# Kernel optimization log

Hardware: AMD Instinct MI355X
Metric: run time of the kernel (lower is better)

## Reference

```python
import jax, jax.numpy as jnp
import numpy as np

DIM_MODEL = 512
HEADS = 8
DIM_HEAD = 64
HIDDEN = HEADS * DIM_HEAD
SCALE = DIM_HEAD ** -0.5
GN_EPS = 1e-5


def setup_inputs() -> dict:
    key = jax.random.key(0)
    ks = jax.random.split(key, 7)
    b, t = 8, 4096
    x = jax.random.normal(ks[0], (b, DIM_MODEL, t), dtype=jnp.float32)
    mask = jax.random.randint(ks[1], (b, t), 0, 2) == 1  # bool padding mask
    # 1x1 convs are plain channel matmuls; kernels squeezed to 2D
    w_qkv = jax.random.normal(ks[2], (3 * HIDDEN, DIM_MODEL), dtype=jnp.float32) * (DIM_MODEL ** -0.5)
    w_out = jax.random.normal(ks[3], (DIM_MODEL, HIDDEN), dtype=jnp.float32) * (HIDDEN ** -0.5)
    b_out = jax.random.normal(ks[4], (DIM_MODEL,), dtype=jnp.float32) * 0.01
    gn_gamma = jnp.ones((DIM_MODEL,), dtype=jnp.float32)
    gn_beta = jnp.zeros((DIM_MODEL,), dtype=jnp.float32)
    return {"x": x, "mask": mask, "w_qkv": w_qkv, "w_out": w_out,
            "b_out": b_out, "gn_gamma": gn_gamma, "gn_beta": gn_beta}


def reference(x, mask, w_qkv, w_out, b_out, gn_gamma, gn_beta):
    b, c, t = x.shape
    # to_qkv: 1x1 conv == channel matmul -> [b, 3*hidden, t]
    qkv = jnp.einsum('oc,bct->bot', w_qkv, x)
    q, k, v = jnp.split(qkv, 3, axis=1)
    # 'b (h d) t -> b h d t'
    q = q.reshape(b, HEADS, DIM_HEAD, t)
    k = k.reshape(b, HEADS, DIM_HEAD, t)
    v = v.reshape(b, HEADS, DIM_HEAD, t)
    # additive mask: 0.0 where True, 1e-12 where False; broadcast 'b t -> b 1 1 t'
    maskf = jnp.where(mask, 0.0, 1e-12)[:, None, None, :].astype(x.dtype)
    q = jax.nn.softmax(q, axis=-2) * SCALE            # softmax over feature dim d
    k = jax.nn.softmax(k + maskf, axis=-1)            # softmax over time dim t
    # linear attention: O(t * d * e)
    context = jnp.einsum('bhdn,bhen->bhde', k, v)      # [b, h, d, e]
    out = jnp.einsum('bhde,bhdn->bhen', context, q)    # [b, h, e, t]
    out = out.reshape(b, HIDDEN, t)                    # 'b h e t -> b (h e) t'
    # to_out: 1x1 conv with bias, then GroupNorm(1, dim_model)
    y = jnp.einsum('oc,bct->bot', w_out, out) + b_out[None, :, None]
    mu = jnp.mean(y, axis=(1, 2), keepdims=True)
    var = jnp.var(y, axis=(1, 2), keepdims=True)
    y = (y - mu) * jax.lax.rsqrt(var + GN_EPS)
    return y * gn_gamma[None, :, None] + gn_beta[None, :, None]
```

## Files before the change

### kernel.cpp

```cpp
#include <hip/hip_runtime.h>
#include <stdint.h>

typedef unsigned short u16;
using f32x4 = __attribute__((ext_vector_type(4))) float;
using s16x8 = __attribute__((ext_vector_type(8))) short;

#define MFMA_BF16(a, b, c) __builtin_amdgcn_mfma_f32_16x16x32_bf16((a), (b), (c), 0, 0, 0)

#define GLOAD_LDS16(gptr, lptr)                                                               \
  __builtin_amdgcn_global_load_lds((const __attribute__((address_space(1))) uint32_t*)(gptr), \
                                   (__attribute__((address_space(3))) uint32_t*)(lptr), 16, 0, 0)

__device__ __forceinline__ u16 f2bf(float f) {
  union { float f; uint32_t u; } v; v.f = f;
  uint32_t r = v.u + 0x7fffu + ((v.u >> 16) & 1u);
  return (u16)(r >> 16);
}
__device__ __forceinline__ float bf2f(u16 h) {
  union { uint32_t u; float f; } v; v.u = ((uint32_t)h) << 16;
  return v.f;
}

__global__ void k_convert_w(const float* __restrict__ wq, const float* __restrict__ wo,
                            u16* __restrict__ wqb, u16* __restrict__ wob) {
  int i = blockIdx.x * 256 + threadIdx.x;
  const int nq = 1536 * 512 / 4;
  const int no = 512 * 512 / 4;
  if (i < nq) {
    float4 v = ((const float4*)wq)[i];
    u16* o = wqb + i * 4;
    o[0] = f2bf(v.x); o[1] = f2bf(v.y); o[2] = f2bf(v.z); o[3] = f2bf(v.w);
  } else if (i < nq + no) {
    int j = i - nq;
    float4 v = ((const float4*)wo)[j];
    u16* o = wob + j * 4;
    o[0] = f2bf(v.x); o[1] = f2bf(v.y); o[2] = f2bf(v.z); o[3] = f2bf(v.w);
  }
}

__global__ void k_transpose_x(const float* __restrict__ x, u16* __restrict__ xT) {
  __shared__ u16 tile[64][65];
  int b = blockIdx.z, c0 = blockIdx.y * 64, t0 = blockIdx.x * 64;
  const float* xp = x + ((size_t)b * 512 + c0) * 4096 + t0;
#pragma unroll
  for (int i = 0; i < 16; ++i) {
    int idx = threadIdx.x + i * 256;
    int r = idx >> 6, col = idx & 63;
    tile[r][col] = f2bf(xp[(size_t)r * 4096 + col]);
  }
  __syncthreads();
  u16* op = xT + ((size_t)b * 4096 + t0) * 512 + c0;
#pragma unroll
  for (int i = 0; i < 16; ++i) {
    int idx = threadIdx.x + i * 256;
    int r = idx >> 6, col = idx & 63;
    op[(size_t)r * 512 + col] = tile[col][r];
  }
}

__launch_bounds__(256, 2)
__global__ void k_gemm_qkv(const u16* __restrict__ A, const u16* __restrict__ BT,
                           u16* __restrict__ C, u16* __restrict__ qT) {
  __shared__ s16x8 As8[1024];
  __shared__ s16x8 Bs8[1024];
  int b = blockIdx.z;
  int m0 = blockIdx.y * 128, n0 = blockIdx.x * 128;
  const u16* Ab = A + (size_t)m0 * 512;
  const u16* Bb = BT + ((size_t)b * 4096 + n0) * 512;
  int tid = threadIdx.x, w = tid >> 6, lane = tid & 63;
  int wm = (w >> 1) * 64, wn = (w & 1) * 64;
  f32x4 acc[4][4] = {};
  for (int kt = 0; kt < 8; ++kt) {
    if (kt) __syncthreads();
#pragma unroll
    for (int it = 0; it < 4; ++it) {
      int L = (w * 4 + it) * 64 + lane;
      int r = L >> 3;
      int lc = (L & 7) ^ (r & 7);
      GLOAD_LDS16(Ab + (size_t)r * 512 + kt * 64 + lc * 8, ((char*)As8) + (w * 4 + it) * 1024);
      GLOAD_LDS16(Bb + (size_t)r * 512 + kt * 64 + lc * 8, ((char*)Bs8) + (w * 4 + it) * 1024);
    }
    asm volatile("s_waitcnt vmcnt(0)");
    __syncthreads();
#pragma unroll
    for (int kk = 0; kk < 2; ++kk) {
      int cb = kk * 4 + (lane >> 4);
      s16x8 af[4], bfr[4];
#pragma unroll
      for (int mi = 0; mi < 4; ++mi) {
        int r = wm + mi * 16 + (lane & 15);
        af[mi] = As8[r * 8 + (cb ^ (r & 7))];
      }
#pragma unroll
      for (int ni = 0; ni < 4; ++ni) {
        int r = wn + ni * 16 + (lane & 15);
        bfr[ni] = Bs8[r * 8 + (cb ^ (r & 7))];
      }
#pragma unroll
      for (int mi = 0; mi < 4; ++mi)
#pragma unroll
        for (int ni = 0; ni < 4; ++ni)
          acc[mi][ni] = MFMA_BF16(af[mi], bfr[ni], acc[mi][ni]);
    }
  }
  if (blockIdx.y < 4) {
    int head = (m0 >> 6) + (wm >> 6);
    int bh = b * 8 + head;
#pragma unroll
    for (int ni = 0; ni < 4; ++ni) {
      float mx = -1e30f;
#pragma unroll
      for (int mi = 0; mi < 4; ++mi)
#pragma unroll
        for (int j = 0; j < 4; ++j) mx = fmaxf(mx, acc[mi][ni][j]);
      mx = fmaxf(mx, __shfl_xor(mx, 16));
      mx = fmaxf(mx, __shfl_xor(mx, 32));
      float e[4][4];
      float s = 0.f;
#pragma unroll
      for (int mi = 0; mi < 4; ++mi)
#pragma unroll
        for (int j = 0; j < 4; ++j) { e[mi][j] = __expf(acc[mi][ni][j] - mx); s += e[mi][j]; }
      s += __shfl_xor(s, 16);
      s += __shfl_xor(s, 32);
      float sc = 0.125f / s;
      int t = n0 + wn + ni * 16 + (lane & 15);
      u16* op = qT + ((size_t)bh * 4096 + t) * 64 + (lane >> 4) * 4;
#pragma unroll
      for (int mi = 0; mi < 4; ++mi) {
        union { u16 u[4]; uint2 v; } pk;
#pragma unroll
        for (int j = 0; j < 4; ++j) pk.u[j] = f2bf(e[mi][j] * sc);
        *(uint2*)(op + mi * 16) = pk.v;
      }
    }
  } else {
    u16* Cb = C + ((size_t)b * 1536 + m0) * 4096 + n0;
#pragma unroll
    for (int mi = 0; mi < 4; ++mi)
#pragma unroll
      for (int ni = 0; ni < 4; ++ni)
#pragma unroll
        for (int j = 0; j < 4; ++j) {
          int mm = wm + mi * 16 + (lane >> 4) * 4 + j;
          int nn = wn + ni * 16 + (lane & 15);
          Cb[(size_t)mm * 4096 + nn] = f2bf(acc[mi][ni][j]);
        }
  }
}

__global__ void k_softmax_k(u16* __restrict__ kp) {
  int row = blockIdx.x;
  int b = row >> 9, rem = row & 511;
  u16* p = kp + ((size_t)b * 1536 + 512 + rem) * 4096;
  int tid = threadIdx.x, lane = tid & 63, w = tid >> 6;
  s16x8 c0 = ((const s16x8*)p)[tid];
  s16x8 c1 = ((const s16x8*)p)[tid + 256];
  float v[16];
#pragma unroll
  for (int j = 0; j < 8; ++j) { v[j] = bf2f((u16)c0[j]); v[8 + j] = bf2f((u16)c1[j]); }
  float mx = -1e30f;
#pragma unroll
  for (int j = 0; j < 16; ++j) mx = fmaxf(mx, v[j]);
#pragma unroll
  for (int off = 32; off; off >>= 1) mx = fmaxf(mx, __shfl_xor(mx, off));
  __shared__ float redm[4], reds[4];
  if (lane == 0) redm[w] = mx;
  __syncthreads();
  mx = fmaxf(fmaxf(redm[0], redm[1]), fmaxf(redm[2], redm[3]));
  float s = 0.f;
#pragma unroll
  for (int j = 0; j < 16; ++j) { v[j] = __expf(v[j] - mx); s += v[j]; }
#pragma unroll
  for (int off = 32; off; off >>= 1) s += __shfl_xor(s, off);
  if (lane == 0) reds[w] = s;
  __syncthreads();
  s = reds[0] + reds[1] + reds[2] + reds[3];
  float inv = 1.f / s;
  s16x8 o0, o1;
#pragma unroll
  for (int j = 0; j < 8; ++j) { o0[j] = (short)f2bf(v[j] * inv); o1[j] = (short)f2bf(v[8 + j] * inv); }
  ((s16x8*)p)[tid] = o0;
  ((s16x8*)p)[tid + 256] = o1;
}

__global__ void k_context_part(const u16* __restrict__ qkv, float* __restrict__ part) {
  int s = blockIdx.x;
  int bh = blockIdx.y;
  int b = bh >> 3, h = bh & 7;
  const u16* vbase = qkv + ((size_t)b * 1536 + 1024 + h * 64) * 4096 + s * 256;
  const u16* kbase = qkv + ((size_t)b * 1536 + 512 + h * 64) * 4096 + s * 256;
  int w = threadIdx.x >> 6, lane = threadIdx.x & 63;
  int e0 = w * 16;
  f32x4 acc[4] = {};
  int er = e0 + (lane & 15);
  int nl = (lane >> 4) * 8;
#pragma unroll
  for (int n0 = 0; n0 < 256; n0 += 32) {
    s16x8 a = *(const s16x8*)(vbase + (size_t)er * 4096 + n0 + nl);
#pragma unroll
    for (int ni = 0; ni < 4; ++ni) {
      s16x8 bb = *(const s16x8*)(kbase + (size_t)(ni * 16 + (lane & 15)) * 4096 + n0 + nl);
      acc[ni] = MFMA_BF16(a, bb, acc[ni]);
    }
  }
  float* cp = part + ((size_t)bh * 16 + s) * 4096;
#pragma unroll
  for (int ni = 0; ni < 4; ++ni)
#pragma unroll
    for (int j = 0; j < 4; ++j) {
      int e = e0 + (lane >> 4) * 4 + j;
      int d = ni * 16 + (lane & 15);
      cp[e * 64 + d] = acc[ni][j];
    }
}

__global__ void k_context_reduce(const float* __restrict__ part, u16* __restrict__ ctxT) {
  int idx = blockIdx.x * 256 + threadIdx.x;
  int bh = idx >> 12, ed = idx & 4095;
  const float* pp = part + (size_t)bh * 16 * 4096 + ed;
  float sum = 0.f;
#pragma unroll
  for (int s = 0; s < 16; ++s) sum += pp[(size_t)s * 4096];
  ctxT[(size_t)bh * 4096 + ed] = f2bf(sum);
}

__launch_bounds__(256, 2)
__global__ void k_attn_out(const u16* __restrict__ qT, const u16* __restrict__ ctxT,
                           u16* __restrict__ outT) {
  __shared__ s16x8 Qs[1024];
  __shared__ s16x8 Cs[512];
  int bh = blockIdx.y;
  int t0 = blockIdx.x * 128;
  int b = bh >> 3, h = bh & 7;
  const u16* qb = qT + ((size_t)bh * 4096 + t0) * 64;
  const u16* cb = ctxT + (size_t)bh * 64 * 64;
  int tid = threadIdx.x, w = tid >> 6, lane = tid & 63;
#pragma unroll
  for (int it = 0; it < 4; ++it) {
    int L = (w * 4 + it) * 64 + lane;
    int r = L >> 3, lc = (L & 7) ^ (r & 7);
    GLOAD_LDS16(qb + (size_t)r * 64 + lc * 8, ((char*)Qs) + (w * 4 + it) * 1024);
  }
#pragma unroll
  for (int it = 0; it < 2; ++it) {
    int L = (w * 2 + it) * 64 + lane;
    int r = L >> 3, lc = (L & 7) ^ (r & 7);
    GLOAD_LDS16(cb + (size_t)r * 64 + lc * 8, ((char*)Cs) + (w * 2 + it) * 1024);
  }
  asm volatile("s_waitcnt vmcnt(0)");
  __syncthreads();
  f32x4 acc[2][4] = {};
#pragma unroll
  for (int kk = 0; kk < 2; ++kk) {
    int cbi = kk * 4 + (lane >> 4);
    s16x8 af[2], bfr[4];
#pragma unroll
    for (int mi = 0; mi < 2; ++mi) {
      int r = w * 32 + mi * 16 + (lane & 15);
      af[mi] = Qs[r * 8 + (cbi ^ (r & 7))];
    }
#pragma unroll
    for (int ni = 0; ni < 4; ++ni) {
      int r = ni * 16 + (lane & 15);
      bfr[ni] = Cs[r * 8 + (cbi ^ (r & 7))];
    }
#pragma unroll
    for (int mi = 0; mi < 2; ++mi)
#pragma unroll
      for (int ni = 0; ni < 4; ++ni)
        acc[mi][ni] = MFMA_BF16(af[mi], bfr[ni], acc[mi][ni]);
  }
  u16* op = outT + ((size_t)b * 4096 + t0) * 512 + h * 64;
#pragma unroll
  for (int mi = 0; mi < 2; ++mi)
#pragma unroll
    for (int ni = 0; ni < 4; ++ni)
#pragma unroll
      for (int j = 0; j < 4; ++j) {
        int t = w * 32 + mi * 16 + (lane >> 4) * 4 + j;
        int e = ni * 16 + (lane & 15);
        op[(size_t)t * 512 + e] = f2bf(acc[mi][ni][j]);
      }
}

__launch_bounds__(256, 2)
__global__ void k_gemm_wout(const u16* __restrict__ A, const u16* __restrict__ BT,
                            u16* __restrict__ Ybf, const float* __restrict__ bias,
                            float2* __restrict__ part2) {
  __shared__ s16x8 As8[1024];
  __shared__ s16x8 Bs8[1024];
  int b = blockIdx.z;
  int m0 = blockIdx.y * 128, n0 = blockIdx.x * 128;
  const u16* Ab = A + (size_t)m0 * 512;
  const u16* Bb = BT + ((size_t)b * 4096 + n0) * 512;
  int tid = threadIdx.x, w = tid >> 6, lane = tid & 63;
  int wm = (w >> 1) * 64, wn = (w & 1) * 64;
  f32x4 acc[4][4] = {};
  for (int kt = 0; kt < 8; ++kt) {
    if (kt) __syncthreads();
#pragma unroll
    for (int it = 0; it < 4; ++it) {
      int L = (w * 4 + it) * 64 + lane;
      int r = L >> 3;
      int lc = (L & 7) ^ (r & 7);
      GLOAD_LDS16(Ab + (size_t)r * 512 + kt * 64 + lc * 8, ((char*)As8) + (w * 4 + it) * 1024);
      GLOAD_LDS16(Bb + (size_t)r * 512 + kt * 64 + lc * 8, ((char*)Bs8) + (w * 4 + it) * 1024);
    }
    asm volatile("s_waitcnt vmcnt(0)");
    __syncthreads();
#pragma unroll
    for (int kk = 0; kk < 2; ++kk) {
      int cb = kk * 4 + (lane >> 4);
      s16x8 af[4], bfr[4];
#pragma unroll
      for (int mi = 0; mi < 4; ++mi) {
        int r = wm + mi * 16 + (lane & 15);
        af[mi] = As8[r * 8 + (cb ^ (r & 7))];
      }
#pragma unroll
      for (int ni = 0; ni < 4; ++ni) {
        int r = wn + ni * 16 + (lane & 15);
        bfr[ni] = Bs8[r * 8 + (cb ^ (r & 7))];
      }
#pragma unroll
      for (int mi = 0; mi < 4; ++mi)
#pragma unroll
        for (int ni = 0; ni < 4; ++ni)
          acc[mi][ni] = MFMA_BF16(af[mi], bfr[ni], acc[mi][ni]);
    }
  }
  u16* Yb = Ybf + ((size_t)b * 512 + m0) * 4096 + n0;
  float sm = 0.f, ssm = 0.f;
#pragma unroll
  for (int mi = 0; mi < 4; ++mi)
#pragma unroll
    for (int j = 0; j < 4; ++j) {
      int mm = wm + mi * 16 + (lane >> 4) * 4 + j;
      float bo = bias[m0 + mm];
#pragma unroll
      for (int ni = 0; ni < 4; ++ni) {
        int nn = wn + ni * 16 + (lane & 15);
        float vv = acc[mi][ni][j] + bo;
        sm += vv;
        ssm += vv * vv;
        Yb[(size_t)mm * 4096 + nn] = f2bf(vv);
      }
    }
#pragma unroll
  for (int off = 32; off; off >>= 1) { sm += __shfl_xor(sm, off); ssm += __shfl_xor(ssm, off); }
  __shared__ float sr[4], ssr[4];
  if (lane == 0) { sr[w] = sm; ssr[w] = ssm; }
  __syncthreads();
  if (tid == 0) {
    float2 o;
    o.x = sr[0] + sr[1] + sr[2] + sr[3];
    o.y = ssr[0] + ssr[1] + ssr[2] + ssr[3];
    part2[((size_t)b * 4 + blockIdx.y) * 32 + blockIdx.x] = o;
  }
}

__global__ void k_gn_norm(const u16* __restrict__ ybf, float* __restrict__ y,
                          const float2* __restrict__ part2,
                          const float* __restrict__ gamma, const float* __restrict__ beta) {
  int b = blockIdx.y;
  float s = 0.f, ss = 0.f;
#pragma unroll 8
  for (int i = 0; i < 128; ++i) { float2 pp = part2[b * 128 + i]; s += pp.x; ss += pp.y; }
  const float N = 512.f * 4096.f;
  float mu = s / N;
  float var = ss / N - mu * mu;
  float rstd = rsqrtf(var + 1e-5f);
  size_t base = ((size_t)b << 21) + (size_t)blockIdx.x * 16384;
  const s16x8* ip = (const s16x8*)(ybf + base);
  float4* opf = (float4*)(y + base);
#pragma unroll
  for (int i = 0; i < 8; ++i) {
    int idx = threadIdx.x + i * 256;
    int loc = (int)(blockIdx.x * 16384) + idx * 8;
    int c = loc >> 12;
    float g = gamma[c] * rstd, bt = beta[c];
    s16x8 v = ip[idx];
    float4 o0, o1;
    o0.x = (bf2f((u16)v[0]) - mu) * g + bt;
    o0.y = (bf2f((u16)v[1]) - mu) * g + bt;
    o0.z = (bf2f((u16)v[2]) - mu) * g + bt;
    o0.w = (bf2f((u16)v[3]) - mu) * g + bt;
    o1.x = (bf2f((u16)v[4]) - mu) * g + bt;
    o1.y = (bf2f((u16)v[5]) - mu) * g + bt;
    o1.z = (bf2f((u16)v[6]) - mu) * g + bt;
    o1.w = (bf2f((u16)v[7]) - mu) * g + bt;
    opf[idx * 2] = o0;
    opf[idx * 2 + 1] = o1;
  }
}

extern "C" void kernel_launch(void* const* d_in, const int* in_sizes, int n_in,
                              void* d_out, int out_size, void* d_ws, size_t ws_size,
                              hipStream_t stream) {
  const float* x     = (const float*)d_in[0];
  const float* wqkv  = (const float*)d_in[2];
  const float* wout  = (const float*)d_in[3];
  const float* bout  = (const float*)d_in[4];
  const float* gamma = (const float*)d_in[5];
  const float* beta  = (const float*)d_in[6];
  float* y = (float*)d_out;

  char* ws = (char*)d_ws;
  u16*    qkv_b = (u16*)ws;
  u16*    ybf   = (u16*)ws;
  u16*    xT    = (u16*)(ws + 100663296);
  u16*    outT  = xT;
  float*  ctxp  = (float*)(ws + 100663296);
  u16*    qT    = (u16*)(ws + 134217728);
  u16*    wqkvb = (u16*)(ws + 167772160);
  u16*    woutb = (u16*)(ws + 169345024);
  u16*    ctxT  = (u16*)(ws + 169869312);
  float2* part2 = (float2*)(ws + 170393600);
  float*  ctxpp = (float*)(ws + 170401792);

  k_convert_w<<<1024, 256, 0, stream>>>(wqkv, wout, wqkvb, woutb);
  {
    dim3 g(64, 8, 8);
    k_transpose_x<<<g, 256, 0, stream>>>(x, xT);
  }
  {
    dim3 g(32, 12, 8);
    k_gemm_qkv<<<g, 256, 0, stream>>>(wqkvb, xT, qkv_b, qT);
  }
  k_softmax_k<<<4096, 256, 0, stream>>>(qkv_b);
  {
    dim3 g(16, 64);
    k_context_part<<<g, 256, 0, stream>>>(qkv_b, ctxpp);
  }
  k_context_reduce<<<1024, 256, 0, stream>>>(ctxpp, ctxT);
  {
    dim3 g(32, 64);
    k_attn_out<<<g, 256, 0, stream>>>(qT, ctxT, outT);
  }
  {
    dim3 g(32, 4, 8);
    k_gemm_wout<<<g, 256, 0, stream>>>(woutb, outT, ybf, bout, part2);
  }
  {
    dim3 g(128, 8);
    k_gn_norm<<<g, 256, 0, stream>>>(ybf, y, part2, gamma, beta);
  }
}
```

Measured before the change: 183.3 us.

## Rewrite QKV and output GEMMs with 128x256 tiles and triple-buffered LDS prefetch

Both 1x1-conv GEMMs now share a macro core that uses 512-thread blocks over 128x256 output tiles, with a 3-stage LDS ring filled by global_load_lds two K-steps ahead. MFMA groups run at raised wave priority and are interleaved with the next stage's loads. The aim is to hide global-load latency behind matrix work, which the old load-wait-compute loop did not do, and to reuse each A tile across a wider N. In exchange the kernels need 144 KB of dynamic LDS, which allows only one block per CU, and launch half as many blocks; the GroupNorm partial-sum layout is adjusted to match.

```diff
diff --git a/kernel.cpp b/kernel.cpp
--- a/kernel.cpp
+++ b/kernel.cpp
@@ -58,53 +58,122 @@
   }
 }
 
-__launch_bounds__(256, 2)
+#define GEMM_CORE_512(Ab, Bb)                                                                  \
+  s16x8* Asl = (s16x8*)lds;                                        \
+  s16x8* Bsl = (s16x8*)(lds + 49152);                              \
+  int tid = threadIdx.x;                                                                       \
+  int w = tid >> 6, lane = tid & 63;                                                           \
+  int wr = w >> 2, wc = w & 3;                                                                 \
+  int hi = lane >> 4, lo = lane & 15;                                                          \
+  int rA = tid >> 3, pc = tid & 7;                                                             \
+  size_t srcA = (size_t)rA * 512 + (size_t)(pc ^ (rA & 7)) * 8;                                \
+  f32x4 acc[4][4] = {};                                                                        \
+        \
+  {                                                                                            \
+    GLOAD_LDS16(Ab + srcA,          ((char*)Asl) + w * 1024);                                  \
+    GLOAD_LDS16(Ab + srcA + 32768,  ((char*)Asl) + 8192 + w * 1024);                           \
+    GLOAD_LDS16(Bb + srcA,          ((char*)Bsl) + w * 1024);                                  \
+    GLOAD_LDS16(Bb + srcA + 32768,  ((char*)Bsl) + 8192 + w * 1024);                           \
+    GLOAD_LDS16(Bb + srcA + 65536,  ((char*)Bsl) + 16384 + w * 1024);                          \
+    GLOAD_LDS16(Bb + srcA + 98304,  ((char*)Bsl) + 24576 + w * 1024);                          \
+    GLOAD_LDS16(Ab + srcA + 64,         ((char*)Asl) + 16384 + w * 1024);                      \
+    GLOAD_LDS16(Ab + srcA + 32768 + 64, ((char*)Asl) + 16384 + 8192 + w * 1024);               \
+    GLOAD_LDS16(Bb + srcA + 64,         ((char*)Bsl) + 32768 + w * 1024);                      \
+    GLOAD_LDS16(Bb + srcA + 32768 + 64, ((char*)Bsl) + 32768 + 8192 + w * 1024);               \
+    GLOAD_LDS16(Bb + srcA + 65536 + 64, ((char*)Bsl) + 32768 + 16384 + w * 1024);              \
+    GLOAD_LDS16(Bb + srcA + 98304 + 64, ((char*)Bsl) + 32768 + 24576 + w * 1024);              \
+  }                                                                                            \
+  int cur = 0;                                                                                 \
+  for (int k = 0; k < 8; ++k) {                                                                \
+    __builtin_amdgcn_sched_barrier(0);                                                         \
+    if (k < 7) { asm volatile("s_waitcnt vmcnt(6)" ::: "memory"); }                            \
+    else       { asm volatile("s_waitcnt vmcnt(0)" ::: "memory"); }                            \
+    __builtin_amdgcn_s_barrier();                                                              \
+    const s16x8* Acur = Asl + cur * 1024;                                                      \
+    const s16x8* Bcur = Bsl + cur * 2048;                                                      \
+    int pt = cur + 2; if (pt >= 3) pt -= 3;                                                    \
+    const u16* Apf = Ab + srcA + (size_t)(k + 2) * 64;                                         \
+    const u16* Bpf = Bb + srcA + (size_t)(k + 2) * 64;                                         \
+    char* Adst = ((char*)Asl) + pt * 16384 + w * 1024;                                         \
+    char* Bdst = ((char*)Bsl) + pt * 32768 + w * 1024;                                         \
+    bool pf = (k < 6);                                                                         \
+                                                                                  \
+    s16x8 af[4][2], bf0[2][2];                                                                 \
+    _Pragma("unroll")                                                                          \
+    for (int mi = 0; mi < 4; ++mi) {                                                           \
+      int r = wr * 64 + mi * 16 + lo;                                                          \
+      _Pragma("unroll")                                                                        \
+      for (int kk = 0; kk < 2; ++kk) {                                                         \
+        int lc = kk * 4 + hi;                                                                  \
+        af[mi][kk] = Acur[r * 8 + (lc ^ (r & 7))];                                             \
+      }                                                                                        \
+    }                                                                                          \
+    _Pragma("unroll")                                                                          \
+    for (int ni = 0; ni < 2; ++ni) {                                                           \
+      int r = wc * 64 + ni * 16 + lo;                                                          \
+      _Pragma("unroll")                                                                        \
+      for (int kk = 0; kk < 2; ++kk) {                                                         \
+        int lc = kk * 4 + hi;                                                                  \
+        bf0[ni][kk] = Bcur[r * 8 + (lc ^ (r & 7))];                                            \
+      }                                                                                        \
+    }                                                                                          \
+    if (pf) {                                                                                  \
+      GLOAD_LDS16(Apf, Adst);                                                                  \
+      GLOAD_LDS16(Apf + 32768, Adst + 8192);                                                   \
+      GLOAD_LDS16(Bpf, Bdst);                                                                  \
+    }                                                                                          \
+    asm volatile("s_waitcnt lgkmcnt(0)" ::: "memory");                                         \
+    __builtin_amdgcn_sched_barrier(0);                                                         \
+    __builtin_amdgcn_s_setprio(1);                                                             \
+    _Pragma("unroll")                                                                          \
+    for (int mi = 0; mi < 4; ++mi)                                                             \
+      _Pragma("unroll")                                                                        \
+      for (int ni = 0; ni < 2; ++ni)                                                           \
+        _Pragma("unroll")                                                                      \
+        for (int kk = 0; kk < 2; ++kk)                                                         \
+          acc[mi][ni] = MFMA_BF16(af[mi][kk], bf0[ni][kk], acc[mi][ni]);                       \
+    __builtin_amdgcn_s_setprio(0);                                                             \
+                                                                                  \
+    s16x8 bf1[2][2];                                                                           \
+    _Pragma("unroll")                                                                          \
+    for (int ni = 0; ni < 2; ++ni) {                                                           \
+      int r = wc * 64 + (ni + 2) * 16 + lo;                                                    \
+      _Pragma("unroll")                                                                        \
+      for (int kk = 0; kk < 2; ++kk) {                                                         \
+        int lc = kk * 4 + hi;                                                                  \
+        bf1[ni][kk] = Bcur[r * 8 + (lc ^ (r & 7))];                                            \
+      }                                                                                        \
+    }                                                                                          \
+    if (pf) {                                                                                  \
+      GLOAD_LDS16(Bpf + 32768, Bdst + 8192);                                                   \
+      GLOAD_LDS16(Bpf + 65536, Bdst + 16384);                                                  \
+      GLOAD_LDS16(Bpf + 98304, Bdst + 24576);                                                  \
+    }                                                                                          \
+    asm volatile("s_waitcnt lgkmcnt(0)" ::: "memory");                                         \
+    __builtin_amdgcn_sched_barrier(0);                                                         \
+    __builtin_amdgcn_s_setprio(1);                                                             \
+    _Pragma("unroll")                                                                          \
+    for (int mi = 0; mi < 4; ++mi)                                                             \
+      _Pragma("unroll")                                                                        \
+      for (int ni = 0; ni < 2; ++ni)                                                           \
+        _Pragma("unroll")                                                                      \
+        for (int kk = 0; kk < 2; ++kk)                                                         \
+          acc[mi][ni + 2] = MFMA_BF16(af[mi][kk], bf1[ni][kk], acc[mi][ni + 2]);               \
+    __builtin_amdgcn_s_setprio(0);                                                             \
+    cur = cur + 1; if (cur == 3) cur = 0;                                                      \
+  }
+
+__launch_bounds__(512, 1)
 __global__ void k_gemm_qkv(const u16* __restrict__ A, const u16* __restrict__ BT,
                            u16* __restrict__ C, u16* __restrict__ qT) {
-  __shared__ s16x8 As8[1024];
-  __shared__ s16x8 Bs8[1024];
+  extern __shared__ char lds[];
   int b = blockIdx.z;
-  int m0 = blockIdx.y * 128, n0 = blockIdx.x * 128;
+  int m0 = blockIdx.y * 128, n0 = blockIdx.x * 256;
   const u16* Ab = A + (size_t)m0 * 512;
   const u16* Bb = BT + ((size_t)b * 4096 + n0) * 512;
-  int tid = threadIdx.x, w = tid >> 6, lane = tid & 63;
-  int wm = (w >> 1) * 64, wn = (w & 1) * 64;
-  f32x4 acc[4][4] = {};
-  for (int kt = 0; kt < 8; ++kt) {
-    if (kt) __syncthreads();
-#pragma unroll
-    for (int it = 0; it < 4; ++it) {
-      int L = (w * 4 + it) * 64 + lane;
-      int r = L >> 3;
-      int lc = (L & 7) ^ (r & 7);
-      GLOAD_LDS16(Ab + (size_t)r * 512 + kt * 64 + lc * 8, ((char*)As8) + (w * 4 + it) * 1024);
-      GLOAD_LDS16(Bb + (size_t)r * 512 + kt * 64 + lc * 8, ((char*)Bs8) + (w * 4 + it) * 1024);
-    }
-    asm volatile("s_waitcnt vmcnt(0)");
-    __syncthreads();
-#pragma unroll
-    for (int kk = 0; kk < 2; ++kk) {
-      int cb = kk * 4 + (lane >> 4);
-      s16x8 af[4], bfr[4];
-#pragma unroll
-      for (int mi = 0; mi < 4; ++mi) {
-        int r = wm + mi * 16 + (lane & 15);
-        af[mi] = As8[r * 8 + (cb ^ (r & 7))];
-      }
-#pragma unroll
-      for (int ni = 0; ni < 4; ++ni) {
-        int r = wn + ni * 16 + (lane & 15);
-        bfr[ni] = Bs8[r * 8 + (cb ^ (r & 7))];
-      }
-#pragma unroll
-      for (int mi = 0; mi < 4; ++mi)
-#pragma unroll
-        for (int ni = 0; ni < 4; ++ni)
-          acc[mi][ni] = MFMA_BF16(af[mi], bfr[ni], acc[mi][ni]);
-    }
-  }
+  GEMM_CORE_512(Ab, Bb)
   if (blockIdx.y < 4) {
-    int head = (m0 >> 6) + (wm >> 6);
+    int head = (int)blockIdx.y * 2 + wr;
     int bh = b * 8 + head;
 #pragma unroll
     for (int ni = 0; ni < 4; ++ni) {
@@ -124,8 +193,8 @@
       s += __shfl_xor(s, 16);
       s += __shfl_xor(s, 32);
       float sc = 0.125f / s;
-      int t = n0 + wn + ni * 16 + (lane & 15);
-      u16* op = qT + ((size_t)bh * 4096 + t) * 64 + (lane >> 4) * 4;
+      int t = n0 + wc * 64 + ni * 16 + lo;
+      u16* op = qT + ((size_t)bh * 4096 + t) * 64 + hi * 4;
 #pragma unroll
       for (int mi = 0; mi < 4; ++mi) {
         union { u16 u[4]; uint2 v; } pk;
@@ -142,10 +211,52 @@
       for (int ni = 0; ni < 4; ++ni)
 #pragma unroll
         for (int j = 0; j < 4; ++j) {
-          int mm = wm + mi * 16 + (lane >> 4) * 4 + j;
-          int nn = wn + ni * 16 + (lane & 15);
+          int mm = wr * 64 + mi * 16 + hi * 4 + j;
+          int nn = wc * 64 + ni * 16 + lo;
           Cb[(size_t)mm * 4096 + nn] = f2bf(acc[mi][ni][j]);
         }
+  }
+}
+
+__launch_bounds__(512, 1)
+__global__ void k_gemm_wout(const u16* __restrict__ A, const u16* __restrict__ BT,
+                            u16* __restrict__ Ybf, const float* __restrict__ bias,
+                            float2* __restrict__ part2) {
+  extern __shared__ char lds[];
+  int b = blockIdx.z;
+  int m0 = blockIdx.y * 128, n0 = blockIdx.x * 256;
+  const u16* Ab = A + (size_t)m0 * 512;
+  const u16* Bb = BT + ((size_t)b * 4096 + n0) * 512;
+  GEMM_CORE_512(Ab, Bb)
+  u16* Yb = Ybf + ((size_t)b * 512 + m0) * 4096 + n0;
+  float sm = 0.f, ssm = 0.f;
+#pragma unroll
+  for (int mi = 0; mi < 4; ++mi)
+#pragma unroll
+    for (int j = 0; j < 4; ++j) {
+      int mm = wr * 64 + mi * 16 + hi * 4 + j;
+      float bo = bias[m0 + mm];
+#pragma unroll
+      for (int ni = 0; ni < 4; ++ni) {
+        int nn = wc * 64 + ni * 16 + lo;
+        float vv = acc[mi][ni][j] + bo;
+        sm += vv;
+        ssm += vv * vv;
+        Yb[(size_t)mm * 4096 + nn] = f2bf(vv);
+      }
+    }
+#pragma unroll
+  for (int off = 32; off; off >>= 1) { sm += __shfl_xor(sm, off); ssm += __shfl_xor(ssm, off); }
+  float* sr = (float*)lds;
+  float* ssr = sr + 8;
+  if (lane == 0) { sr[w] = sm; ssr[w] = ssm; }
+  __syncthreads();
+  if (tid == 0) {
+    float2 o;
+    o.x = 0.f; o.y = 0.f;
+#pragma unroll
+    for (int i = 0; i < 8; ++i) { o.x += sr[i]; o.y += ssr[i]; }
+    part2[((size_t)b * 4 + blockIdx.y) * 16 + blockIdx.x] = o;
   }
 }
 
@@ -284,89 +395,13 @@
       }
 }
 
-__launch_bounds__(256, 2)
-__global__ void k_gemm_wout(const u16* __restrict__ A, const u16* __restrict__ BT,
-                            u16* __restrict__ Ybf, const float* __restrict__ bias,
-                            float2* __restrict__ part2) {
-  __shared__ s16x8 As8[1024];
-  __shared__ s16x8 Bs8[1024];
-  int b = blockIdx.z;
-  int m0 = blockIdx.y * 128, n0 = blockIdx.x * 128;
-  const u16* Ab = A + (size_t)m0 * 512;
-  const u16* Bb = BT + ((size_t)b * 4096 + n0) * 512;
-  int tid = threadIdx.x, w = tid >> 6, lane = tid & 63;
-  int wm = (w >> 1) * 64, wn = (w & 1) * 64;
-  f32x4 acc[4][4] = {};
-  for (int kt = 0; kt < 8; ++kt) {
-    if (kt) __syncthreads();
-#pragma unroll
-    for (int it = 0; it < 4; ++it) {
-      int L = (w * 4 + it) * 64 + lane;
-      int r = L >> 3;
-      int lc = (L & 7) ^ (r & 7);
-      GLOAD_LDS16(Ab + (size_t)r * 512 + kt * 64 + lc * 8, ((char*)As8) + (w * 4 + it) * 1024);
-      GLOAD_LDS16(Bb + (size_t)r * 512 + kt * 64 + lc * 8, ((char*)Bs8) + (w * 4 + it) * 1024);
-    }
-    asm volatile("s_waitcnt vmcnt(0)");
-    __syncthreads();
-#pragma unroll
-    for (int kk = 0; kk < 2; ++kk) {
-      int cb = kk * 4 + (lane >> 4);
-      s16x8 af[4], bfr[4];
-#pragma unroll
-      for (int mi = 0; mi < 4; ++mi) {
-        int r = wm + mi * 16 + (lane & 15);
-        af[mi] = As8[r * 8 + (cb ^ (r & 7))];
-      }
-#pragma unroll
-      for (int ni = 0; ni < 4; ++ni) {
-        int r = wn + ni * 16 + (lane & 15);
-        bfr[ni] = Bs8[r * 8 + (cb ^ (r & 7))];
-      }
-#pragma unroll
-      for (int mi = 0; mi < 4; ++mi)
-#pragma unroll
-        for (int ni = 0; ni < 4; ++ni)
-          acc[mi][ni] = MFMA_BF16(af[mi], bfr[ni], acc[mi][ni]);
-    }
-  }
-  u16* Yb = Ybf + ((size_t)b * 512 + m0) * 4096 + n0;
-  float sm = 0.f, ssm = 0.f;
-#pragma unroll
-  for (int mi = 0; mi < 4; ++mi)
-#pragma unroll
-    for (int j = 0; j < 4; ++j) {
-      int mm = wm + mi * 16 + (lane >> 4) * 4 + j;
-      float bo = bias[m0 + mm];
-#pragma unroll
-      for (int ni = 0; ni < 4; ++ni) {
-        int nn = wn + ni * 16 + (lane & 15);
-        float vv = acc[mi][ni][j] + bo;
-        sm += vv;
-        ssm += vv * vv;
-        Yb[(size_t)mm * 4096 + nn] = f2bf(vv);
-      }
-    }
-#pragma unroll
-  for (int off = 32; off; off >>= 1) { sm += __shfl_xor(sm, off); ssm += __shfl_xor(ssm, off); }
-  __shared__ float sr[4], ssr[4];
-  if (lane == 0) { sr[w] = sm; ssr[w] = ssm; }
-  __syncthreads();
-  if (tid == 0) {
-    float2 o;
-    o.x = sr[0] + sr[1] + sr[2] + sr[3];
-    o.y = ssr[0] + ssr[1] + ssr[2] + ssr[3];
-    part2[((size_t)b * 4 + blockIdx.y) * 32 + blockIdx.x] = o;
-  }
-}
-
 __global__ void k_gn_norm(const u16* __restrict__ ybf, float* __restrict__ y,
                           const float2* __restrict__ part2,
                           const float* __restrict__ gamma, const float* __restrict__ beta) {
   int b = blockIdx.y;
   float s = 0.f, ss = 0.f;
 #pragma unroll 8
-  for (int i = 0; i < 128; ++i) { float2 pp = part2[b * 128 + i]; s += pp.x; ss += pp.y; }
+  for (int i = 0; i < 64; ++i) { float2 pp = part2[b * 64 + i]; s += pp.x; ss += pp.y; }
   const float N = 512.f * 4096.f;
   float mu = s / N;
   float var = ss / N - mu * mu;
@@ -411,7 +446,6 @@
   u16*    ybf   = (u16*)ws;
   u16*    xT    = (u16*)(ws + 100663296);
   u16*    outT  = xT;
-  float*  ctxp  = (float*)(ws + 100663296);
   u16*    qT    = (u16*)(ws + 134217728);
   u16*    wqkvb = (u16*)(ws + 167772160);
   u16*    woutb = (u16*)(ws + 169345024);
@@ -419,14 +453,20 @@
   float2* part2 = (float2*)(ws + 170393600);
   float*  ctxpp = (float*)(ws + 170401792);
 
+  const int GEMM_LDS = 147456;
+  (void)hipFuncSetAttribute((const void*)k_gemm_qkv,
+                            hipFuncAttributeMaxDynamicSharedMemorySize, GEMM_LDS);
+  (void)hipFuncSetAttribute((const void*)k_gemm_wout,
+                            hipFuncAttributeMaxDynamicSharedMemorySize, GEMM_LDS);
+
   k_convert_w<<<1024, 256, 0, stream>>>(wqkv, wout, wqkvb, woutb);
   {
     dim3 g(64, 8, 8);
     k_transpose_x<<<g, 256, 0, stream>>>(x, xT);
   }
   {
-    dim3 g(32, 12, 8);
-    k_gemm_qkv<<<g, 256, 0, stream>>>(wqkvb, xT, qkv_b, qT);
+    dim3 g(16, 12, 8);
+    k_gemm_qkv<<<g, 512, GEMM_LDS, stream>>>(wqkvb, xT, qkv_b, qT);
   }
   k_softmax_k<<<4096, 256, 0, stream>>>(qkv_b);
   {
@@ -439,8 +479,8 @@
     k_attn_out<<<g, 256, 0, stream>>>(qT, ctxT, outT);
   }
   {
-    dim3 g(32, 4, 8);
-    k_gemm_wout<<<g, 256, 0, stream>>>(woutb, outT, ybf, bout, part2);
+    dim3 g(16, 4, 8);
+    k_gemm_wout<<<g, 512, GEMM_LDS, stream>>>(woutb, outT, ybf, bout, part2);
   }
   {
     dim3 g(128, 8);
```

Result: faster. 179.3 us (-2.2%).

## Fold context into output weights and fuse k-softmax into context accumulation

Applied to the files above, without the earlier changes.

Removes the separate k-softmax pass. The exponentials are now computed inside the context-partial kernel, with per-row sums reduced alongside it and normalization applied during the context reduction. The per-(batch,head) context is folded into w_out to build a per-batch fused weight, so the final GEMM reads q directly and the attn_out kernel and its intermediate buffer go away. The exp is taken without max subtraction, which risks overflow on large k values, and the fused weight is rounded to bf16, which adds some precision error.

```diff
diff --git a/kernel.cpp b/kernel.cpp
--- a/kernel.cpp
+++ b/kernel.cpp
@@ -149,151 +149,110 @@
   }
 }
 
-__global__ void k_softmax_k(u16* __restrict__ kp) {
-  int row = blockIdx.x;
-  int b = row >> 9, rem = row & 511;
-  u16* p = kp + ((size_t)b * 1536 + 512 + rem) * 4096;
-  int tid = threadIdx.x, lane = tid & 63, w = tid >> 6;
-  s16x8 c0 = ((const s16x8*)p)[tid];
-  s16x8 c1 = ((const s16x8*)p)[tid + 256];
-  float v[16];
-#pragma unroll
-  for (int j = 0; j < 8; ++j) { v[j] = bf2f((u16)c0[j]); v[8 + j] = bf2f((u16)c1[j]); }
-  float mx = -1e30f;
-#pragma unroll
-  for (int j = 0; j < 16; ++j) mx = fmaxf(mx, v[j]);
-#pragma unroll
-  for (int off = 32; off; off >>= 1) mx = fmaxf(mx, __shfl_xor(mx, off));
-  __shared__ float redm[4], reds[4];
-  if (lane == 0) redm[w] = mx;
+__global__ void k_context_part(const u16* __restrict__ qkv, float* __restrict__ ctxp,
+                               float* __restrict__ spart) {
+  int s = blockIdx.x, bh = blockIdx.y;
+  int b = bh >> 3, h = bh & 7;
+  int w = threadIdx.x >> 6, lane = threadIdx.x & 63;
+  int hi = lane >> 4, lo = lane & 15;
+  const u16* vb = qkv + ((size_t)b * 1536 + 1024 + h * 64) * 4096 + s * 256;
+  const u16* kb = qkv + ((size_t)b * 1536 + 512 + h * 64) * 4096 + s * 256;
+  int d = w * 16 + lo;
+  f32x4 acc[4] = {};
+  float ssum = 0.f;
+#pragma unroll
+  for (int st = 0; st < 8; ++st) {
+    int nn = st * 32 + hi * 8;
+    s16x8 braw = *(const s16x8*)(kb + (size_t)d * 4096 + nn);
+    s16x8 bexp;
+#pragma unroll
+    for (int j = 0; j < 8; ++j) {
+      float f = __expf(bf2f((u16)braw[j]));
+      ssum += f;
+      bexp[j] = (short)f2bf(f);
+    }
+#pragma unroll
+    for (int ei = 0; ei < 4; ++ei) {
+      s16x8 a = *(const s16x8*)(vb + (size_t)(ei * 16 + lo) * 4096 + nn);
+      acc[ei] = MFMA_BF16(a, bexp, acc[ei]);
+    }
+  }
+  float* cp = ctxp + ((size_t)bh * 16 + s) * 4096;
+#pragma unroll
+  for (int ei = 0; ei < 4; ++ei) {
+    float4 o;
+    o.x = acc[ei][0]; o.y = acc[ei][1]; o.z = acc[ei][2]; o.w = acc[ei][3];
+    *(float4*)&cp[(size_t)d * 64 + ei * 16 + hi * 4] = o;
+  }
+  ssum += __shfl_xor(ssum, 16);
+  ssum += __shfl_xor(ssum, 32);
+  if (lane < 16) spart[((size_t)bh * 16 + s) * 64 + w * 16 + lane] = ssum;
+}
+
+__global__ void k_ctx_reduce(const float* __restrict__ ctxp, const float* __restrict__ spart,
+                             u16* __restrict__ Bg) {
+  int q = blockIdx.x, bh = blockIdx.y;
+  __shared__ float sinv[4];
+  int tid = threadIdx.x;
+  if (tid < 4) {
+    int d = q * 4 + tid;
+    float s = 0.f;
+#pragma unroll
+    for (int si = 0; si < 16; ++si) s += spart[((size_t)bh * 16 + si) * 64 + d];
+    sinv[tid] = 1.f / s;
+  }
   __syncthreads();
-  mx = fmaxf(fmaxf(redm[0], redm[1]), fmaxf(redm[2], redm[3]));
-  float s = 0.f;
-#pragma unroll
-  for (int j = 0; j < 16; ++j) { v[j] = __expf(v[j] - mx); s += v[j]; }
-#pragma unroll
-  for (int off = 32; off; off >>= 1) s += __shfl_xor(s, off);
-  if (lane == 0) reds[w] = s;
-  __syncthreads();
-  s = reds[0] + reds[1] + reds[2] + reds[3];
-  float inv = 1.f / s;
-  s16x8 o0, o1;
-#pragma unroll
-  for (int j = 0; j < 8; ++j) { o0[j] = (short)f2bf(v[j] * inv); o1[j] = (short)f2bf(v[8 + j] * inv); }
-  ((s16x8*)p)[tid] = o0;
-  ((s16x8*)p)[tid + 256] = o1;
-}
-
-__global__ void k_context_part(const u16* __restrict__ qkv, float* __restrict__ part) {
-  int s = blockIdx.x;
-  int bh = blockIdx.y;
+  int pos = q * 256 + tid;
+  float v = 0.f;
+#pragma unroll
+  for (int si = 0; si < 16; ++si) v += ctxp[((size_t)bh * 16 + si) * 4096 + pos];
+  Bg[(size_t)bh * 4096 + pos] = f2bf(v * sinv[(pos >> 6) & 3]);
+}
+
+__global__ void k_wfused(const u16* __restrict__ wout, const u16* __restrict__ Bg,
+                         u16* __restrict__ Wf) {
+  int bh = blockIdx.x;
   int b = bh >> 3, h = bh & 7;
-  const u16* vbase = qkv + ((size_t)b * 1536 + 1024 + h * 64) * 4096 + s * 256;
-  const u16* kbase = qkv + ((size_t)b * 1536 + 512 + h * 64) * 4096 + s * 256;
   int w = threadIdx.x >> 6, lane = threadIdx.x & 63;
-  int e0 = w * 16;
-  f32x4 acc[4] = {};
-  int er = e0 + (lane & 15);
-  int nl = (lane >> 4) * 8;
-#pragma unroll
-  for (int n0 = 0; n0 < 256; n0 += 32) {
-    s16x8 a = *(const s16x8*)(vbase + (size_t)er * 4096 + n0 + nl);
+  int hi = lane >> 4, lo = lane & 15;
+  const u16* Bb = Bg + (size_t)bh * 4096;
+  const u16* Ab = wout + (size_t)h * 64;
+  f32x4 acc[8][4] = {};
+#pragma unroll
+  for (int ks = 0; ks < 2; ++ks) {
+    s16x8 bfr[4];
+#pragma unroll
+    for (int ni = 0; ni < 4; ++ni)
+      bfr[ni] = *(const s16x8*)(Bb + (size_t)(ni * 16 + lo) * 64 + ks * 32 + hi * 8);
+#pragma unroll
+    for (int mi = 0; mi < 8; ++mi) {
+      s16x8 a = *(const s16x8*)(Ab + (size_t)(w * 128 + mi * 16 + lo) * 512 + ks * 32 + hi * 8);
+#pragma unroll
+      for (int ni = 0; ni < 4; ++ni) acc[mi][ni] = MFMA_BF16(a, bfr[ni], acc[mi][ni]);
+    }
+  }
+#pragma unroll
+  for (int mi = 0; mi < 8; ++mi)
 #pragma unroll
     for (int ni = 0; ni < 4; ++ni) {
-      s16x8 bb = *(const s16x8*)(kbase + (size_t)(ni * 16 + (lane & 15)) * 4096 + n0 + nl);
-      acc[ni] = MFMA_BF16(a, bb, acc[ni]);
-    }
-  }
-  float* cp = part + ((size_t)bh * 16 + s) * 4096;
-#pragma unroll
-  for (int ni = 0; ni < 4; ++ni)
-#pragma unroll
-    for (int j = 0; j < 4; ++j) {
-      int e = e0 + (lane >> 4) * 4 + j;
-      int d = ni * 16 + (lane & 15);
-      cp[e * 64 + d] = acc[ni][j];
-    }
-}
-
-__global__ void k_context_reduce(const float* __restrict__ part, u16* __restrict__ ctxT) {
-  int idx = blockIdx.x * 256 + threadIdx.x;
-  int bh = idx >> 12, ed = idx & 4095;
-  const float* pp = part + (size_t)bh * 16 * 4096 + ed;
-  float sum = 0.f;
-#pragma unroll
-  for (int s = 0; s < 16; ++s) sum += pp[(size_t)s * 4096];
-  ctxT[(size_t)bh * 4096 + ed] = f2bf(sum);
+      int m = w * 128 + mi * 16 + hi * 4;
+      int d = ni * 16 + lo;
+#pragma unroll
+      for (int j = 0; j < 4; ++j)
+        Wf[((size_t)b * 512 + m + j) * 512 + h * 64 + d] = f2bf(acc[mi][ni][j]);
+    }
 }
 
 __launch_bounds__(256, 2)
-__global__ void k_attn_out(const u16* __restrict__ qT, const u16* __restrict__ ctxT,
-                           u16* __restrict__ outT) {
-  __shared__ s16x8 Qs[1024];
-  __shared__ s16x8 Cs[512];
-  int bh = blockIdx.y;
-  int t0 = blockIdx.x * 128;
-  int b = bh >> 3, h = bh & 7;
-  const u16* qb = qT + ((size_t)bh * 4096 + t0) * 64;
-  const u16* cb = ctxT + (size_t)bh * 64 * 64;
-  int tid = threadIdx.x, w = tid >> 6, lane = tid & 63;
-#pragma unroll
-  for (int it = 0; it < 4; ++it) {
-    int L = (w * 4 + it) * 64 + lane;
-    int r = L >> 3, lc = (L & 7) ^ (r & 7);
-    GLOAD_LDS16(qb + (size_t)r * 64 + lc * 8, ((char*)Qs) + (w * 4 + it) * 1024);
-  }
-#pragma unroll
-  for (int it = 0; it < 2; ++it) {
-    int L = (w * 2 + it) * 64 + lane;
-    int r = L >> 3, lc = (L & 7) ^ (r & 7);
-    GLOAD_LDS16(cb + (size_t)r * 64 + lc * 8, ((char*)Cs) + (w * 2 + it) * 1024);
-  }
-  asm volatile("s_waitcnt vmcnt(0)");
-  __syncthreads();
-  f32x4 acc[2][4] = {};
-#pragma unroll
-  for (int kk = 0; kk < 2; ++kk) {
-    int cbi = kk * 4 + (lane >> 4);
-    s16x8 af[2], bfr[4];
-#pragma unroll
-    for (int mi = 0; mi < 2; ++mi) {
-      int r = w * 32 + mi * 16 + (lane & 15);
-      af[mi] = Qs[r * 8 + (cbi ^ (r & 7))];
-    }
-#pragma unroll
-    for (int ni = 0; ni < 4; ++ni) {
-      int r = ni * 16 + (lane & 15);
-      bfr[ni] = Cs[r * 8 + (cbi ^ (r & 7))];
-    }
-#pragma unroll
-    for (int mi = 0; mi < 2; ++mi)
-#pragma unroll
-      for (int ni = 0; ni < 4; ++ni)
-        acc[mi][ni] = MFMA_BF16(af[mi], bfr[ni], acc[mi][ni]);
-  }
-  u16* op = outT + ((size_t)b * 4096 + t0) * 512 + h * 64;
-#pragma unroll
-  for (int mi = 0; mi < 2; ++mi)
-#pragma unroll
-    for (int ni = 0; ni < 4; ++ni)
-#pragma unroll
-      for (int j = 0; j < 4; ++j) {
-        int t = w * 32 + mi * 16 + (lane >> 4) * 4 + j;
-        int e = ni * 16 + (lane & 15);
-        op[(size_t)t * 512 + e] = f2bf(acc[mi][ni][j]);
-      }
-}
-
-__launch_bounds__(256, 2)
-__global__ void k_gemm_wout(const u16* __restrict__ A, const u16* __restrict__ BT,
-                            u16* __restrict__ Ybf, const float* __restrict__ bias,
-                            float2* __restrict__ part2) {
+__global__ void k_gemm_final(const u16* __restrict__ Wf, const u16* __restrict__ qT,
+                             u16* __restrict__ Ybf, const float* __restrict__ bias,
+                             float2* __restrict__ part2) {
   __shared__ s16x8 As8[1024];
   __shared__ s16x8 Bs8[1024];
   int b = blockIdx.z;
   int m0 = blockIdx.y * 128, n0 = blockIdx.x * 128;
-  const u16* Ab = A + (size_t)m0 * 512;
-  const u16* Bb = BT + ((size_t)b * 4096 + n0) * 512;
+  const u16* Ab = Wf + ((size_t)b * 512 + m0) * 512;
+  const u16* qTb = qT + (size_t)b * 8 * 4096 * 64;
   int tid = threadIdx.x, w = tid >> 6, lane = tid & 63;
   int wm = (w >> 1) * 64, wn = (w & 1) * 64;
   f32x4 acc[4][4] = {};
@@ -305,7 +264,9 @@
       int r = L >> 3;
       int lc = (L & 7) ^ (r & 7);
       GLOAD_LDS16(Ab + (size_t)r * 512 + kt * 64 + lc * 8, ((char*)As8) + (w * 4 + it) * 1024);
-      GLOAD_LDS16(Bb + (size_t)r * 512 + kt * 64 + lc * 8, ((char*)Bs8) + (w * 4 + it) * 1024);
+      int G = kt * 8 + lc;
+      GLOAD_LDS16(qTb + ((size_t)(G >> 3) * 4096 + n0 + r) * 64 + (G & 7) * 8,
+                  ((char*)Bs8) + (w * 4 + it) * 1024);
     }
     asm volatile("s_waitcnt vmcnt(0)");
     __syncthreads();
@@ -410,14 +371,14 @@
   u16*    qkv_b = (u16*)ws;
   u16*    ybf   = (u16*)ws;
   u16*    xT    = (u16*)(ws + 100663296);
-  u16*    outT  = xT;
   float*  ctxp  = (float*)(ws + 100663296);
+  float*  spart = (float*)(ws + 117440512);
+  u16*    Bg    = (u16*)(ws + 117702656);
   u16*    qT    = (u16*)(ws + 134217728);
   u16*    wqkvb = (u16*)(ws + 167772160);
   u16*    woutb = (u16*)(ws + 169345024);
-  u16*    ctxT  = (u16*)(ws + 169869312);
-  float2* part2 = (float2*)(ws + 170393600);
-  float*  ctxpp = (float*)(ws + 170401792);
+  u16*    Wfused= (u16*)(ws + 169869312);
+  float2* part2 = (float2*)(ws + 174063616);
 
   k_convert_w<<<1024, 256, 0, stream>>>(wqkv, wout, wqkvb, woutb);
   {
@@ -428,19 +389,18 @@
     dim3 g(32, 12, 8);
     k_gemm_qkv<<<g, 256, 0, stream>>>(wqkvb, xT, qkv_b, qT);
   }
-  k_softmax_k<<<4096, 256, 0, stream>>>(qkv_b);
   {
     dim3 g(16, 64);
-    k_context_part<<<g, 256, 0, stream>>>(qkv_b, ctxpp);
-  }
-  k_context_reduce<<<1024, 256, 0, stream>>>(ctxpp, ctxT);
-  {
-    dim3 g(32, 64);
-    k_attn_out<<<g, 256, 0, stream>>>(qT, ctxT, outT);
-  }
+    k_context_part<<<g, 256, 0, stream>>>(qkv_b, ctxp, spart);
+  }
+  {
+    dim3 g(16, 64);
+    k_ctx_reduce<<<g, 256, 0, stream>>>(ctxp, spart, Bg);
+  }
+  k_wfused<<<64, 256, 0, stream>>>(woutb, Bg, Wfused);
   {
     dim3 g(32, 4, 8);
-    k_gemm_wout<<<g, 256, 0, stream>>>(woutb, outT, ybf, bout, part2);
+    k_gemm_final<<<g, 256, 0, stream>>>(Wfused, qT, ybf, bout, part2);
   }
   {
     dim3 g(128, 8);
```

Result: faster. 177.9 us (-2.9%).
